# Optimization experiments

Hardware: AMD Instinct MI355X
Metric: run time of the kernel (lower is better)

Reference implementation:

```python
import jax, jax.numpy as jnp
import numpy as np

# ---- configuration (matches init_kwargs / dg) ----
B, N, C = 8192, 64, 8           # batch, n columns, per-column cardinality
D = N * C                        # 512, concatenated one-hot width
HP, HS = 1024, 512
TAU = 0.7
SMOOTH = 0.1                     # kwargs['smoothing'] (truthy -> smoothing branch taken)
CAUSAL_COLS = (0, 5, 10)         # dg.causal_cols
PARENT, CHILD, REL_TYPE = 2, 7, 0  # dg.binary_relations


def _lin(k, fan_in, shape):
    return jax.random.normal(k, shape, dtype=jnp.float32) * np.float32(1.0 / np.sqrt(fan_in))


def setup_inputs() -> dict:
    key = jax.random.key(0)
    ks = jax.random.split(key, 16)
    # x / truth_x are concatenations of N one-hot columns of cardinality C
    x = jax.nn.one_hot(jax.random.randint(ks[0], (B, N), 0, C), C, dtype=jnp.float32).reshape(B, D)
    truth_x = jax.nn.one_hot(jax.random.randint(ks[1], (B, N), 0, C), C, dtype=jnp.float32).reshape(B, D)
    return {
        'x': x, 'truth_x': truth_x,
        # selector: Linear(D,HS) -> ReLU -> Linear(HS,N) -> Sigmoid
        'sel_w1': _lin(ks[2], D, (D, HS)), 'sel_b1': jnp.zeros((HS,), jnp.float32),
        'sel_w2': _lin(ks[3], HS, (HS, N)), 'sel_b2': jnp.zeros((N,), jnp.float32),
        # perturber: Linear(D,HP) -> ReLU -> Linear(HP,HP) -> ReLU -> Linear(HP,HP) -> ReLU -> Linear(HP,D)
        'pw1': _lin(ks[4], D, (D, HP)),  'pb1': jnp.zeros((HP,), jnp.float32),
        'pw2': _lin(ks[5], HP, (HP, HP)), 'pb2': jnp.zeros((HP,), jnp.float32),
        'pw3': _lin(ks[6], HP, (HP, HP)), 'pb3': jnp.zeros((HP,), jnp.float32),
        'pw4': _lin(ks[7], HP, (HP, D)),  'pb4': jnp.zeros((D,), jnp.float32),
    }


def _gumbel_softmax_smoothed(logits, noise):
    # torch: pr = (1-s)*softmax(logits) + s/c ; logits = log(pr); gumbel_softmax(logits, tau, hard=False)
    pr = jax.nn.softmax(logits, axis=-1)
    pr = (1.0 - SMOOTH) * pr + SMOOTH / C
    return jax.nn.softmax((jnp.log(pr) + noise) / TAU, axis=-1)


def reference(x, truth_x, sel_w1, sel_b1, sel_w2, sel_b2,
              pw1, pb1, pw2, pb2, pw3, pb3, pw4, pb4):
    key = jax.random.key(42)
    ka, kb, kg = jax.random.split(key, 3)

    # selector -> P in (0,1), shape [B, N]
    P = jax.nn.sigmoid(jnp.maximum(x @ sel_w1 + sel_b1, 0.0) @ sel_w2 + sel_b2)

    # relaxed Bernoulli (training branch of Sample_Bernoulli)
    ua = jax.random.uniform(ka, (B, N), dtype=x.dtype, minval=1e-8, maxval=1.0)
    ub = jax.random.uniform(kb, (B, N), dtype=x.dtype, minval=1e-8, maxval=1.0)
    ea = jnp.exp(-jnp.log(-jnp.log(ua)))
    eb = jnp.exp(-jnp.log(-jnp.log(ub)))
    no = P * ea / TAU
    de = no + (1.0 - P) * eb / TAU
    probs = no / de                                   # [B, N]

    # perturber MLP -> per-column logits W, shape [B, D]
    h = jnp.maximum(x @ pw1 + pb1, 0.0)
    h = jnp.maximum(h @ pw2 + pb2, 0.0)
    h = jnp.maximum(h @ pw3 + pb3, 0.0)
    W = h @ pw4 + pb4

    x3 = x.reshape(B, N, C)
    W3 = W.reshape(B, N, C)
    curr = jnp.argmax(x3, axis=-1)                    # [B, N] current states
    g = -jnp.log(-jnp.log(jax.random.uniform(kg, (B, N, C), dtype=x.dtype,
                                             minval=1e-8, maxval=1.0)))  # shared Gumbel noise

    # ---- pass 1: PARENT column (unmasked) to determine increasing/constant samples ----
    xt_par = _gumbel_softmax_smoothed(W3[:, PARENT], g[:, PARENT])
    p_par = probs[:, PARENT, None]
    out_par = p_par * xt_par + (1.0 - p_par) * x3[:, PARENT]
    diff = jnp.argmax(out_par, axis=-1) - curr[:, PARENT]
    const = diff == 0
    incr = diff > 0

    # ---- probability adjustments for CHILD column ----
    p_child = probs[:, CHILD] * (1.0 - const.astype(probs.dtype))  # zero on constant samples
    if REL_TYPE == 0:
        p_child = jnp.clip(p_child + incr.astype(probs.dtype), 0.0, 1.0)
    p2 = probs.at[:, CHILD].set(p_child)

    # ---- additive logit masks (torch adds ones everywhere, -100 on forbidden states) ----
    ar = jnp.arange(C)
    addmask = jnp.zeros((B, N, C), dtype=x.dtype)
    for i in CAUSAL_COLS:  # all rows are "samples"; mask states < curr
        addmask = addmask.at[:, i].set(
            jnp.where(ar[None, :] < curr[:, i, None], -100.0, 1.0))
    thr = curr[:, CHILD, None] + (1 if REL_TYPE == 0 else 0)
    addmask = addmask.at[:, CHILD].set(
        jnp.where(incr[:, None] & (ar[None, :] < thr), -100.0, 1.0))

    # ---- all columns, vectorized (same Gumbel noise as pass 1 for the parent) ----
    xt = _gumbel_softmax_smoothed(W3 + addmask, g)    # [B, N, C]
    out = p2[:, :, None] * xt + (1.0 - p2[:, :, None]) * x3
    xcf = out.reshape(B, D)

    return (truth_x, xcf, P, W)
```

## Files before the change

kernel.cpp:

```cpp
#include <hip/hip_runtime.h>
#include <stdint.h>

#define BB 8192
#define NN 64
#define CC 8
#define DD 512
#define HPP 1024
#define HSS 512

typedef _Float16 f16x8 __attribute__((ext_vector_type(8)));
typedef float f32x4 __attribute__((ext_vector_type(4)));

__host__ __device__ __forceinline__ void threefry2x32(
    uint32_t k0, uint32_t k1, uint32_t x0, uint32_t x1,
    uint32_t& o0, uint32_t& o1)
{
  const uint32_t ks2 = k0 ^ k1 ^ 0x1BD11BDAu;
#define TFR(r) { x0 += x1; x1 = (x1 << (r)) | (x1 >> (32 - (r))); x1 ^= x0; }
  x0 += k0; x1 += k1;
  TFR(13) TFR(15) TFR(26) TFR(6)
  x0 += k1;  x1 += ks2 + 1u;
  TFR(17) TFR(29) TFR(16) TFR(24)
  x0 += ks2; x1 += k0 + 2u;
  TFR(13) TFR(15) TFR(26) TFR(6)
  x0 += k0;  x1 += k1 + 3u;
  TFR(17) TFR(29) TFR(16) TFR(24)
  x0 += k1;  x1 += ks2 + 4u;
  TFR(13) TFR(15) TFR(26) TFR(6)
  x0 += ks2; x1 += k0 + 5u;
#undef TFR
  o0 = x0; o1 = x1;
}

__device__ __forceinline__ uint32_t tf_bits_p(uint32_t k0, uint32_t k1,
                                              uint32_t idx)
{
  uint32_t o0, o1;
  threefry2x32(k0, k1, 0u, idx, o0, o1);
  return o0 ^ o1;
}

__device__ __forceinline__ float jax_uniform(uint32_t bits)
{
  const float f = __uint_as_float((bits >> 9) | 0x3f800000u) - 1.0f;
  return fmaxf(1e-8f, f + 1e-8f);
}

__device__ __forceinline__ int kswz(int k, int r)
{
  return (k & ~31) | ((((k >> 3) ^ (r >> 1)) & 3) << 3) | (k & 7);
}

__device__ __forceinline__ void async_copy16(void* lds, const void* g)
{
  __builtin_amdgcn_global_load_lds(
      (const __attribute__((address_space(1))) unsigned int*)g,
      (__attribute__((address_space(3))) unsigned int*)lds,
      16, 0, 0);
}

template<int ROWS>
__device__ __forceinline__ void stage_tile(_Float16* lds, const _Float16* g,
                                           int row0, int ldK, int k0, int tid)
{
  constexpr int SLOTS = ROWS * 4;
#pragma unroll
  for (int s0 = 0; s0 < SLOTS; s0 += 256) {
    const int s = s0 + tid;
    const char* gp = (const char*)(g + (size_t)(row0 + (s >> 2)) * ldK + k0)
                     + (s & 3) * 16;
    async_copy16((char*)lds + (size_t)s * 16, gp);
  }
}

__device__ __forceinline__ f16x8 frag_ld(const _Float16* base, int row, int lk)
{
  const int off = row * 32 + (((lk ^ (row >> 1)) & 3) << 3);
  return *(const f16x8*)(base + off);
}

template<int BM, int BN, int ALO, int EPI>
__global__ __launch_bounds__(256, 2)
void gemm_mfma(const _Float16* __restrict__ Ahi, const _Float16* __restrict__ Alo,
               const _Float16* __restrict__ BhiT, const _Float16* __restrict__ BloT,
               const float* __restrict__ bias,
               _Float16* __restrict__ ChiOut, _Float16* __restrict__ CloOut,
               float* __restrict__ Cf32,
               int M, int N, int K)
{
  __shared__ __align__(16) _Float16 As_hi[BM * 32];
  __shared__ __align__(16) _Float16 As_lo[ALO ? BM * 32 : 8];
  __shared__ __align__(16) _Float16 Bs_hi[BN * 32];
  __shared__ __align__(16) _Float16 Bs_lo[BN * 32];

  const int tid = threadIdx.x;
  const int wid = tid >> 6, lane = tid & 63;
  const int wr = wid >> 1, wc = wid & 1;
  constexpr int WROWS = BM / 2, WCOLS = BN / 2;
  constexpr int FRM = WROWS / 16, FRN = WCOLS / 16;
  const int lr = lane & 15, lk = lane >> 4;

  const int gx = gridDim.x;
  const int nwg = gx * gridDim.y;
  int lin = blockIdx.x + blockIdx.y * gx;
  if ((nwg & 7) == 0) {
    const int chunk = nwg >> 3;
    lin = (lin & 7) * chunk + (lin >> 3);
  }
  const int bn = (lin % gx) * BN;
  const int bm = (lin / gx) * BM;

  f32x4 acc[FRM][FRN] = {};

  for (int k0 = 0; k0 < K; k0 += 32) {
    __syncthreads();
    stage_tile<BM>(As_hi, Ahi, bm, K, k0, tid);
    if (ALO) stage_tile<BM>(As_lo, Alo, bm, K, k0, tid);
    stage_tile<BN>(Bs_hi, BhiT, bn, K, k0, tid);
    stage_tile<BN>(Bs_lo, BloT, bn, K, k0, tid);
    __syncthreads();

    f16x8 ah[FRM], al[FRM], bh[FRN], bl[FRN];
#pragma unroll
    for (int m = 0; m < FRM; ++m) {
      const int r = wr * WROWS + m * 16 + lr;
      ah[m] = frag_ld(As_hi, r, lk);
      if (ALO) al[m] = frag_ld(As_lo, r, lk);
    }
#pragma unroll
    for (int n = 0; n < FRN; ++n) {
      const int r = wc * WCOLS + n * 16 + lr;
      bh[n] = frag_ld(Bs_hi, r, lk);
      bl[n] = frag_ld(Bs_lo, r, lk);
    }
#pragma unroll
    for (int m = 0; m < FRM; ++m)
#pragma unroll
      for (int n = 0; n < FRN; ++n) {
        acc[m][n] = __builtin_amdgcn_mfma_f32_16x16x32_f16(ah[m], bh[n], acc[m][n], 0, 0, 0);
        acc[m][n] = __builtin_amdgcn_mfma_f32_16x16x32_f16(ah[m], bl[n], acc[m][n], 0, 0, 0);
        if (ALO)
          acc[m][n] = __builtin_amdgcn_mfma_f32_16x16x32_f16(al[m], bh[n], acc[m][n], 0, 0, 0);
      }
  }

  float bvals[FRN];
#pragma unroll
  for (int n = 0; n < FRN; ++n)
    bvals[n] = bias[bn + wc * WCOLS + n * 16 + lr];

#pragma unroll
  for (int m = 0; m < FRM; ++m)
#pragma unroll
    for (int n = 0; n < FRN; ++n)
#pragma unroll
      for (int q = 0; q < 4; ++q) {
        const int R = bm + wr * WROWS + m * 16 + lk * 4 + q;
        const int Cc = bn + wc * WCOLS + n * 16 + lr;
        float v = acc[m][n][q] + bvals[n];
        if (EPI == 0) {
          v = fmaxf(v, 0.0f);
          const _Float16 h = (_Float16)v;
          const _Float16 l = (_Float16)(v - (float)h);
          const size_t off = (size_t)R * N + kswz(Cc, R);
          ChiOut[off] = h;
          CloOut[off] = l;
        } else if (EPI == 1) {
          Cf32[(size_t)R * N + Cc] = 1.0f / (1.0f + expf(-v));
        } else {
          Cf32[(size_t)R * N + Cc] = v;
        }
      }
}

__global__ __launch_bounds__(256)
void wconv(const float* __restrict__ w, _Float16* __restrict__ hiT,
           _Float16* __restrict__ loT, int K, int N)
{
  __shared__ float tile[64][65];
  const int n0 = blockIdx.x * 64, k0 = blockIdx.y * 64;
  const int t = threadIdx.x;
  const int c = t & 63, r4 = t >> 6;
#pragma unroll
  for (int i = 0; i < 16; ++i) {
    const int r = r4 * 16 + i;
    tile[r][c] = w[(size_t)(k0 + r) * N + n0 + c];
  }
  __syncthreads();
#pragma unroll
  for (int i = 0; i < 16; ++i) {
    const int n = r4 * 16 + i;
    const int k = c;
    const float v = tile[k][n];
    const _Float16 h = (_Float16)v;
    const _Float16 l = (_Float16)(v - (float)h);
    const int R = n0 + n;
    const size_t off = (size_t)R * K + kswz(k0 + k, R);
    hiT[off] = h;
    loT[off] = l;
  }
}

__global__ __launch_bounds__(256)
void xconv(const float* __restrict__ x, _Float16* __restrict__ hi)
{
  const int gid = blockIdx.x * 256 + threadIdx.x;
  const int R = gid >> 6, slot = gid & 63;
  const float4* p = (const float4*)(x + (size_t)R * 512 + slot * 8);
  const float4 a = p[0], b = p[1];
  f16x8 h;
  h[0] = (_Float16)a.x; h[1] = (_Float16)a.y; h[2] = (_Float16)a.z; h[3] = (_Float16)a.w;
  h[4] = (_Float16)b.x; h[5] = (_Float16)b.y; h[6] = (_Float16)b.z; h[7] = (_Float16)b.w;
  const int chunk = (slot >> 2) << 5;
  const int s = (slot & 3) ^ ((R >> 1) & 3);
  *(f16x8*)(hi + (size_t)R * 512 + chunk + s * 8) = h;
}

__global__ __launch_bounds__(256)
void finalize_kernel(const float* __restrict__ x,
                     const float* __restrict__ truth,
                     const float* __restrict__ Pm,
                     const float* __restrict__ Wm,
                     float* __restrict__ o_truth,
                     float* __restrict__ o_xcf,
                     uint32_t ka0, uint32_t ka1,
                     uint32_t kb0, uint32_t kb1,
                     uint32_t kg0, uint32_t kg1)
{
  const int gid = blockIdx.x * 256 + threadIdx.x;
  const int b = gid >> 6;
  const int n = gid & 63;
  const size_t ro = (size_t)b * DD + (size_t)n * CC;

  {
    float4 t0 = *reinterpret_cast<const float4*>(truth + ro);
    float4 t1 = *reinterpret_cast<const float4*>(truth + ro + 4);
    *reinterpret_cast<float4*>(o_truth + ro) = t0;
    *reinterpret_cast<float4*>(o_truth + ro + 4) = t1;
  }

  float x8[8];
  {
    float4 a = *reinterpret_cast<const float4*>(x + ro);
    float4 c = *reinterpret_cast<const float4*>(x + ro + 4);
    x8[0] = a.x; x8[1] = a.y; x8[2] = a.z; x8[3] = a.w;
    x8[4] = c.x; x8[5] = c.y; x8[6] = c.z; x8[7] = c.w;
  }
  int curr = 0;
  {
    float xm = x8[0];
#pragma unroll
    for (int c = 1; c < 8; ++c) if (x8[c] > xm) { xm = x8[c]; curr = c; }
  }

  const uint32_t ia = (uint32_t)(b * NN + n);
  const float ua = jax_uniform(tf_bits_p(ka0, ka1, ia));
  const float ub = jax_uniform(tf_bits_p(kb0, kb1, ia));
  const float eaa = expf(-logf(-logf(ua)));
  const float ebb = expf(-logf(-logf(ub)));
  const float Pv = Pm[(size_t)b * NN + n];
  const float no = Pv * eaa / 0.7f;
  const float de = no + (1.0f - Pv) * ebb / 0.7f;
  const float prob = no / de;

  float g8[8];
#pragma unroll
  for (int c = 0; c < 8; ++c)
    g8[c] = -logf(-logf(jax_uniform(tf_bits_p(kg0, kg1, ia * 8u + (uint32_t)c))));

  float w8[8];
  {
    float4 a = *reinterpret_cast<const float4*>(Wm + ro);
    float4 c = *reinterpret_cast<const float4*>(Wm + ro + 4);
    w8[0] = a.x; w8[1] = a.y; w8[2] = a.z; w8[3] = a.w;
    w8[4] = c.x; w8[5] = c.y; w8[6] = c.z; w8[7] = c.w;
  }

  int diff = 0;
  if (n == 2) {
    float mx = w8[0];
#pragma unroll
    for (int c = 1; c < 8; ++c) mx = fmaxf(mx, w8[c]);
    float e[8], s = 0.0f;
#pragma unroll
    for (int c = 0; c < 8; ++c) { e[c] = expf(w8[c] - mx); s += e[c]; }
    float l2[8];
#pragma unroll
    for (int c = 0; c < 8; ++c)
      l2[c] = (logf(0.9f * (e[c] / s) + 0.0125f) + g8[c]) / 0.7f;
    float mx2 = l2[0];
#pragma unroll
    for (int c = 1; c < 8; ++c) mx2 = fmaxf(mx2, l2[c]);
    float e2[8], s2 = 0.0f;
#pragma unroll
    for (int c = 0; c < 8; ++c) { e2[c] = expf(l2[c] - mx2); s2 += e2[c]; }
    float bv = -1e30f; int am = 0;
#pragma unroll
    for (int c = 0; c < 8; ++c) {
      float ov = prob * (e2[c] / s2) + (1.0f - prob) * x8[c];
      if (ov > bv) { bv = ov; am = c; }
    }
    diff = am - curr;
  }
  diff = __shfl(diff, 2, 64);
  const bool cst = (diff == 0);
  const bool inc = (diff > 0);

  float p2 = prob;
  if (n == 7) {
    float pc = prob * (cst ? 0.0f : 1.0f) + (inc ? 1.0f : 0.0f);
    p2 = fminf(fmaxf(pc, 0.0f), 1.0f);
  }

  const bool causal = (n == 0) | (n == 5) | (n == 10);
  float lg[8];
#pragma unroll
  for (int c = 0; c < 8; ++c) {
    float m = 0.0f;
    if (causal) m = (c < curr) ? -100.0f : 1.0f;
    if (n == 7) m = (inc && (c < curr + 1)) ? -100.0f : 1.0f;
    lg[c] = w8[c] + m;
  }

  float mx = lg[0];
#pragma unroll
  for (int c = 1; c < 8; ++c) mx = fmaxf(mx, lg[c]);
  float e[8], s = 0.0f;
#pragma unroll
  for (int c = 0; c < 8; ++c) { e[c] = expf(lg[c] - mx); s += e[c]; }
  float l2[8];
#pragma unroll
  for (int c = 0; c < 8; ++c)
    l2[c] = (logf(0.9f * (e[c] / s) + 0.0125f) + g8[c]) / 0.7f;
  float mx2 = l2[0];
#pragma unroll
  for (int c = 1; c < 8; ++c) mx2 = fmaxf(mx2, l2[c]);
  float e2[8], s2 = 0.0f;
#pragma unroll
  for (int c = 0; c < 8; ++c) { e2[c] = expf(l2[c] - mx2); s2 += e2[c]; }

  float4 o0, o1;
  float* op = &o0.x;
#pragma unroll
  for (int c = 0; c < 4; ++c) op[c] = p2 * (e2[c] / s2) + (1.0f - p2) * x8[c];
  float* op1 = &o1.x;
#pragma unroll
  for (int c = 0; c < 4; ++c) op1[c] = p2 * (e2[c + 4] / s2) + (1.0f - p2) * x8[c + 4];
  *reinterpret_cast<float4*>(o_xcf + ro) = o0;
  *reinterpret_cast<float4*>(o_xcf + ro + 4) = o1;
}

extern "C" void kernel_launch(void* const* d_in, const int* in_sizes, int n_in,
                              void* d_out, int out_size, void* d_ws, size_t ws_size,
                              hipStream_t stream)
{
  const float* x     = (const float*)d_in[0];
  const float* truth = (const float*)d_in[1];
  const float* sw1   = (const float*)d_in[2];
  const float* sb1   = (const float*)d_in[3];
  const float* sw2   = (const float*)d_in[4];
  const float* sb2   = (const float*)d_in[5];
  const float* pw1   = (const float*)d_in[6];
  const float* pb1   = (const float*)d_in[7];
  const float* pw2   = (const float*)d_in[8];
  const float* pb2   = (const float*)d_in[9];
  const float* pw3   = (const float*)d_in[10];
  const float* pb3   = (const float*)d_in[11];
  const float* pw4   = (const float*)d_in[12];
  const float* pb4   = (const float*)d_in[13];

  float* out      = (float*)d_out;
  float* o_truth  = out;
  float* o_xcf    = out + (size_t)BB * DD;
  float* o_P      = o_xcf + (size_t)BB * DD;
  float* o_W      = o_P + (size_t)BB * NN;

  _Float16* wsb = (_Float16*)d_ws;
  size_t cur = 0;
  auto alloc = [&](size_t nelem) { _Float16* p = wsb + cur; cur += nelem; return p; };
  _Float16* sw1T_hi = alloc(512 * 512);   _Float16* sw1T_lo = alloc(512 * 512);
  _Float16* sw2T_hi = alloc(64 * 512);    _Float16* sw2T_lo = alloc(64 * 512);
  _Float16* pw1T_hi = alloc(1024 * 512);  _Float16* pw1T_lo = alloc(1024 * 512);
  _Float16* pw2T_hi = alloc(1024 * 1024); _Float16* pw2T_lo = alloc(1024 * 1024);
  _Float16* pw3T_hi = alloc(1024 * 1024); _Float16* pw3T_lo = alloc(1024 * 1024);
  _Float16* pw4T_hi = alloc(512 * 1024);  _Float16* pw4T_lo = alloc(512 * 1024);
  _Float16* R1 = alloc((size_t)16 * 1024 * 1024);
  _Float16* x_hi  = R1;
  _Float16* s1_hi = R1 + (size_t)BB * HSS;
  _Float16* s1_lo = s1_hi + (size_t)BB * HSS;
  _Float16* h2_hi = R1;
  _Float16* h2_lo = R1 + (size_t)BB * HPP;
  _Float16* h1_hi = (_Float16*)d_out;
  _Float16* h1_lo = h1_hi + (size_t)BB * HPP;
  _Float16* h3_hi = h1_hi;
  _Float16* h3_lo = h1_lo;

  uint32_t ka0, ka1, kb0, kb1, kg0, kg1;
  threefry2x32(0u, 42u, 0u, 0u, ka0, ka1);
  threefry2x32(0u, 42u, 0u, 1u, kb0, kb1);
  threefry2x32(0u, 42u, 0u, 2u, kg0, kg1);

  dim3 blk(256);

  wconv<<<dim3(512 / 64, 512 / 64), blk, 0, stream>>>(sw1, sw1T_hi, sw1T_lo, 512, 512);
  wconv<<<dim3(64 / 64, 512 / 64), blk, 0, stream>>>(sw2, sw2T_hi, sw2T_lo, 512, 64);
  wconv<<<dim3(1024 / 64, 512 / 64), blk, 0, stream>>>(pw1, pw1T_hi, pw1T_lo, 512, 1024);
  wconv<<<dim3(1024 / 64, 1024 / 64), blk, 0, stream>>>(pw2, pw2T_hi, pw2T_lo, 1024, 1024);
  wconv<<<dim3(1024 / 64, 1024 / 64), blk, 0, stream>>>(pw3, pw3T_hi, pw3T_lo, 1024, 1024);
  wconv<<<dim3(512 / 64, 1024 / 64), blk, 0, stream>>>(pw4, pw4T_hi, pw4T_lo, 1024, 512);
  xconv<<<dim3(BB * 64 / 256), blk, 0, stream>>>(x, x_hi);

  gemm_mfma<128, 128, 0, 0><<<dim3(HSS / 128, BB / 128), blk, 0, stream>>>(
      x_hi, nullptr, sw1T_hi, sw1T_lo, sb1, s1_hi, s1_lo, nullptr, BB, HSS, DD);
  gemm_mfma<128, 64, 1, 1><<<dim3(NN / 64, BB / 128), blk, 0, stream>>>(
      s1_hi, s1_lo, sw2T_hi, sw2T_lo, sb2, nullptr, nullptr, o_P, BB, NN, HSS);
  gemm_mfma<128, 128, 0, 0><<<dim3(HPP / 128, BB / 128), blk, 0, stream>>>(
      x_hi, nullptr, pw1T_hi, pw1T_lo, pb1, h1_hi, h1_lo, nullptr, BB, HPP, DD);
  gemm_mfma<128, 128, 1, 0><<<dim3(HPP / 128, BB / 128), blk, 0, stream>>>(
      h1_hi, h1_lo, pw2T_hi, pw2T_lo, pb2, h2_hi, h2_lo, nullptr, BB, HPP, HPP);
  gemm_mfma<128, 128, 1, 0><<<dim3(HPP / 128, BB / 128), blk, 0, stream>>>(
      h2_hi, h2_lo, pw3T_hi, pw3T_lo, pb3, h3_hi, h3_lo, nullptr, BB, HPP, HPP);
  gemm_mfma<128, 128, 1, 2><<<dim3(DD / 128, BB / 128), blk, 0, stream>>>(
      h3_hi, h3_lo, pw4T_hi, pw4T_lo, pb4, nullptr, nullptr, o_W, BB, DD, HPP);

  finalize_kernel<<<dim3(BB * NN / 256), blk, 0, stream>>>(
      x, truth, o_P, o_W, o_truth, o_xcf,
      ka0, ka1, kb0, kb1, kg0, kg1);
}
```

Before: 354.6 us.

## Fuse selector and perturber first-layer GEMMs and shrink GEMM tiles to 128x64

Both first-layer GEMMs read x, so their transposed weights are concatenated into one 1536-wide B matrix and computed in a single launch. A new epilogue mode routes columns below 512 to the selector hidden buffer and the rest to the perturber hidden buffer, each with its own bias. All big GEMMs switch from 128x128 to 128x64 tiles and launch_bounds asks for 4 blocks per CU, giving more workgroups and higher occupancy. The cost is less operand reuse per tile, more A-matrix traffic, and register pressure that may cause spills.

```diff
diff --git a/kernel.cpp b/kernel.cpp
--- a/kernel.cpp
+++ b/kernel.cpp
@@ -80,13 +80,15 @@
 }
 
 template<int BM, int BN, int ALO, int EPI>
-__global__ __launch_bounds__(256, 2)
+__global__ __launch_bounds__(256, 4)
 void gemm_mfma(const _Float16* __restrict__ Ahi, const _Float16* __restrict__ Alo,
                const _Float16* __restrict__ BhiT, const _Float16* __restrict__ BloT,
                const float* __restrict__ bias,
                _Float16* __restrict__ ChiOut, _Float16* __restrict__ CloOut,
                float* __restrict__ Cf32,
-               int M, int N, int K)
+               int M, int N, int K,
+               const float* __restrict__ bias2,
+               _Float16* __restrict__ Chi2, _Float16* __restrict__ Clo2)
 {
   __shared__ __align__(16) _Float16 As_hi[BM * 32];
   __shared__ __align__(16) _Float16 As_lo[ALO ? BM * 32 : 8];
@@ -144,20 +146,18 @@
       }
   }
 
-  float bvals[FRN];
-#pragma unroll
-  for (int n = 0; n < FRN; ++n)
-    bvals[n] = bias[bn + wc * WCOLS + n * 16 + lr];
-
 #pragma unroll
   for (int m = 0; m < FRM; ++m)
 #pragma unroll
-    for (int n = 0; n < FRN; ++n)
+    for (int n = 0; n < FRN; ++n) {
+      const int Cc = bn + wc * WCOLS + n * 16 + lr;
+      float bv;
+      if (EPI == 3) bv = (Cc < 512) ? bias[Cc] : bias2[Cc - 512];
+      else          bv = bias[Cc];
 #pragma unroll
       for (int q = 0; q < 4; ++q) {
         const int R = bm + wr * WROWS + m * 16 + lk * 4 + q;
-        const int Cc = bn + wc * WCOLS + n * 16 + lr;
-        float v = acc[m][n][q] + bvals[n];
+        float v = acc[m][n][q] + bv;
         if (EPI == 0) {
           v = fmaxf(v, 0.0f);
           const _Float16 h = (_Float16)v;
@@ -167,10 +167,25 @@
           CloOut[off] = l;
         } else if (EPI == 1) {
           Cf32[(size_t)R * N + Cc] = 1.0f / (1.0f + expf(-v));
+        } else if (EPI == 2) {
+          Cf32[(size_t)R * N + Cc] = v;
         } else {
-          Cf32[(size_t)R * N + Cc] = v;
+          v = fmaxf(v, 0.0f);
+          const _Float16 h = (_Float16)v;
+          const _Float16 l = (_Float16)(v - (float)h);
+          if (Cc < 512) {
+            const size_t off = (size_t)R * 512 + kswz(Cc, R);
+            ChiOut[off] = h;
+            CloOut[off] = l;
+          } else {
+            const int c2 = Cc - 512;
+            const size_t off = (size_t)R * 1024 + kswz(c2, R);
+            Chi2[off] = h;
+            Clo2[off] = l;
+          }
         }
       }
+    }
 }
 
 __global__ __launch_bounds__(256)
@@ -378,9 +393,9 @@
   _Float16* wsb = (_Float16*)d_ws;
   size_t cur = 0;
   auto alloc = [&](size_t nelem) { _Float16* p = wsb + cur; cur += nelem; return p; };
-  _Float16* sw1T_hi = alloc(512 * 512);   _Float16* sw1T_lo = alloc(512 * 512);
+  _Float16* sB_hi  = alloc((size_t)1536 * 512);
+  _Float16* sB_lo  = alloc((size_t)1536 * 512);
   _Float16* sw2T_hi = alloc(64 * 512);    _Float16* sw2T_lo = alloc(64 * 512);
-  _Float16* pw1T_hi = alloc(1024 * 512);  _Float16* pw1T_lo = alloc(1024 * 512);
   _Float16* pw2T_hi = alloc(1024 * 1024); _Float16* pw2T_lo = alloc(1024 * 1024);
   _Float16* pw3T_hi = alloc(1024 * 1024); _Float16* pw3T_lo = alloc(1024 * 1024);
   _Float16* pw4T_hi = alloc(512 * 1024);  _Float16* pw4T_lo = alloc(512 * 1024);
@@ -402,26 +417,30 @@
 
   dim3 blk(256);
 
-  wconv<<<dim3(512 / 64, 512 / 64), blk, 0, stream>>>(sw1, sw1T_hi, sw1T_lo, 512, 512);
+  wconv<<<dim3(512 / 64, 512 / 64), blk, 0, stream>>>(sw1, sB_hi, sB_lo, 512, 512);
+  wconv<<<dim3(1024 / 64, 512 / 64), blk, 0, stream>>>(
+      pw1, sB_hi + (size_t)512 * 512, sB_lo + (size_t)512 * 512, 512, 1024);
   wconv<<<dim3(64 / 64, 512 / 64), blk, 0, stream>>>(sw2, sw2T_hi, sw2T_lo, 512, 64);
-  wconv<<<dim3(1024 / 64, 512 / 64), blk, 0, stream>>>(pw1, pw1T_hi, pw1T_lo, 512, 1024);
   wconv<<<dim3(1024 / 64, 1024 / 64), blk, 0, stream>>>(pw2, pw2T_hi, pw2T_lo, 1024, 1024);
   wconv<<<dim3(1024 / 64, 1024 / 64), blk, 0, stream>>>(pw3, pw3T_hi, pw3T_lo, 1024, 1024);
   wconv<<<dim3(512 / 64, 1024 / 64), blk, 0, stream>>>(pw4, pw4T_hi, pw4T_lo, 1024, 512);
   xconv<<<dim3(BB * 64 / 256), blk, 0, stream>>>(x, x_hi);
 
-  gemm_mfma<128, 128, 0, 0><<<dim3(HSS / 128, BB / 128), blk, 0, stream>>>(
-      x_hi, nullptr, sw1T_hi, sw1T_lo, sb1, s1_hi, s1_lo, nullptr, BB, HSS, DD);
+  gemm_mfma<128, 64, 0, 3><<<dim3(1536 / 64, BB / 128), blk, 0, stream>>>(
+      x_hi, nullptr, sB_hi, sB_lo, sb1, s1_hi, s1_lo, nullptr, BB, 1536, DD,
+      pb1, h1_hi, h1_lo);
   gemm_mfma<128, 64, 1, 1><<<dim3(NN / 64, BB / 128), blk, 0, stream>>>(
-      s1_hi, s1_lo, sw2T_hi, sw2T_lo, sb2, nullptr, nullptr, o_P, BB, NN, HSS);
-  gemm_mfma<128, 128, 0, 0><<<dim3(HPP / 128, BB / 128), blk, 0, stream>>>(
-      x_hi, nullptr, pw1T_hi, pw1T_lo, pb1, h1_hi, h1_lo, nullptr, BB, HPP, DD);
-  gemm_mfma<128, 128, 1, 0><<<dim3(HPP / 128, BB / 128), blk, 0, stream>>>(
-      h1_hi, h1_lo, pw2T_hi, pw2T_lo, pb2, h2_hi, h2_lo, nullptr, BB, HPP, HPP);
-  gemm_mfma<128, 128, 1, 0><<<dim3(HPP / 128, BB / 128), blk, 0, stream>>>(
-      h2_hi, h2_lo, pw3T_hi, pw3T_lo, pb3, h3_hi, h3_lo, nullptr, BB, HPP, HPP);
-  gemm_mfma<128, 128, 1, 2><<<dim3(DD / 128, BB / 128), blk, 0, stream>>>(
-      h3_hi, h3_lo, pw4T_hi, pw4T_lo, pb4, nullptr, nullptr, o_W, BB, DD, HPP);
+      s1_hi, s1_lo, sw2T_hi, sw2T_lo, sb2, nullptr, nullptr, o_P, BB, NN, HSS,
+      nullptr, nullptr, nullptr);
+  gemm_mfma<128, 64, 1, 0><<<dim3(HPP / 64, BB / 128), blk, 0, stream>>>(
+      h1_hi, h1_lo, pw2T_hi, pw2T_lo, pb2, h2_hi, h2_lo, nullptr, BB, HPP, HPP,
+      nullptr, nullptr, nullptr);
+  gemm_mfma<128, 64, 1, 0><<<dim3(HPP / 64, BB / 128), blk, 0, stream>>>(
+      h2_hi, h2_lo, pw3T_hi, pw3T_lo, pb3, h3_hi, h3_lo, nullptr, BB, HPP, HPP,
+      nullptr, nullptr, nullptr);
+  gemm_mfma<128, 64, 1, 2><<<dim3(DD / 64, BB / 128), blk, 0, stream>>>(
+      h3_hi, h3_lo, pw4T_hi, pw4T_lo, pb4, nullptr, nullptr, o_W, BB, DD, HPP,
+      nullptr, nullptr, nullptr);
 
   finalize_kernel<<<dim3(BB * NN / 256), blk, 0, stream>>>(
       x, truth, o_P, o_W, o_truth, o_xcf,
```

After: 366.8 us. 1.03x slower.
